# Performance work log

Measured on AMD Instinct MI355X. Metric: run time of the kernel, lower is better.

## Reference

```python
import jax, jax.numpy as jnp
import numpy as np

N_HEADS = 8
WINDOW = 7

def _conv1x1(x, W, b):
    # x: [B,H,W,C]; 1x1 conv == per-pixel matmul
    return jnp.einsum('bhwc,cd->bhwd', x, W) + b

def _to_heads(t, nh):
    # [B,H,W,C] -> channels-first reshape [B, nh, C//nh, H*W] (matches tf transpose+reshape)
    B, H, W, C = t.shape
    return jnp.transpose(t, (0, 3, 1, 2)).reshape(B, nh, C // nh, H * W)

def setup_inputs() -> dict:
    key = jax.random.key(0)
    ks = jax.random.split(key, 8)
    B, H, W, C = 2, 56, 56, 256
    x = jax.random.normal(ks[0], (B, H, W, C), dtype=jnp.float32)
    s = 1.0 / np.sqrt(C)
    Wq = jax.random.normal(ks[1], (C, C), dtype=jnp.float32) * s
    bq = jnp.zeros((C,), dtype=jnp.float32)
    Wk = jax.random.normal(ks[2], (C, C), dtype=jnp.float32) * s
    bk = jnp.zeros((C,), dtype=jnp.float32)
    Wv = jax.random.normal(ks[3], (C, C), dtype=jnp.float32) * s
    bv = jnp.zeros((C,), dtype=jnp.float32)
    # original initializes gamma to 0 (output == x); use small nonzero so the
    # attention path is observable in outputs/grads
    gamma = jax.random.normal(ks[4], (1,), dtype=jnp.float32) * 0.1
    return {"x": x, "Wq": Wq, "bq": bq, "Wk": Wk, "bk": bk, "Wv": Wv, "bv": bv, "gamma": gamma}

def reference(x, Wq, bq, Wk, bk, Wv, bv, gamma):
    B, H, W, C = x.shape
    p = WINDOW // 2
    xp = jnp.pad(x, ((0, 0), (p, p), (p, p), (0, 0)), mode='reflect')  # [B,Hp,Wp,C]
    q = _to_heads(_conv1x1(x, Wq, bq), N_HEADS)    # [B,nh,dk,HW]
    k = _to_heads(_conv1x1(xp, Wk, bk), N_HEADS)   # [B,nh,dk,HpWp]
    v = _to_heads(_conv1x1(xp, Wv, bv), N_HEADS)   # [B,nh,dk,HpWp]
    energy = jnp.einsum('bhdq,bhdk->bhqk', q, k)   # [B,nh,HW,HpWp]
    attn = jax.nn.softmax(energy, axis=-1)
    out = jnp.einsum('bhdk,bhqk->bhdq', v, attn)   # [B,nh,dk,HW]
    out = out.reshape(B, C, H, W).transpose(0, 2, 3, 1)
    return gamma * out + x
```

## Files before the change

### kernel.cpp

```cpp
#include <hip/hip_runtime.h>

typedef unsigned short u16;
typedef float f32x4 __attribute__((ext_vector_type(4)));
typedef short bf16x8 __attribute__((ext_vector_type(8)));

__device__ __forceinline__ u16 f2bf(float f) {
    unsigned u = __float_as_uint(f);
    u = (u + 0x7FFFu + ((u >> 16) & 1u)) >> 16;
    return (u16)u;
}

#define LOG2E 1.4426950408889634f

#if __has_builtin(__builtin_amdgcn_exp2f)
__device__ __forceinline__ float exp2_fast(float x) { return __builtin_amdgcn_exp2f(x); }
#else
__device__ __forceinline__ float exp2_fast(float x) { return __expf(x * 0.6931471805599453f); }
#endif

__device__ __forceinline__ unsigned pack2bf(float a, float b) {
    unsigned ua = __float_as_uint(a) + 0x8000u;
    unsigned ub = __float_as_uint(b) + 0x8000u;
#if __has_builtin(__builtin_amdgcn_perm)
    return __builtin_amdgcn_perm(ub, ua, 0x07060302u);
#else
    return ((ua >> 16) & 0xFFFFu) | (ub & 0xFFFF0000u);
#endif
}

#if __has_builtin(__builtin_amdgcn_cvt_pk_bf16_f32)
typedef __bf16 bf2_t __attribute__((ext_vector_type(2)));
__device__ __forceinline__ unsigned cvtpk(float a, float b) {
    bf2_t r = __builtin_amdgcn_cvt_pk_bf16_f32(a, b);
    return __builtin_bit_cast(unsigned, r);
}
#else
__device__ __forceinline__ unsigned cvtpk(float a, float b) { return pack2bf(a, b); }
#endif

__device__ __forceinline__ bf16x8 bc8(uint4 u) { return __builtin_bit_cast(bf16x8, u); }

#if __has_builtin(__builtin_amdgcn_global_load_lds)
typedef const __attribute__((address_space(1))) void* as1cv;
typedef __attribute__((address_space(3))) void* as3v;
__device__ __forceinline__ void dma16(const void* g, void* lds_base, int lane) {
    __builtin_amdgcn_global_load_lds((as1cv)g, (as3v)lds_base, 16, 0, 0);
}
#else
__device__ __forceinline__ void dma16(const void* g, void* lds_base, int lane) {
    *(uint4*)((char*)lds_base + lane * 16) = *(const uint4*)g;
}
#endif

#define BB 2
#define HH 56
#define SQ 3136
#define CROWN 3584

#define WS_Q    0
#define WS_K    1605632
#define WS_V    3244032
#define WS_WT   4882432
#define WS_CB   5079040
#define WS_XB   5082624

__global__ __launch_bounds__(256) void prep_kernel(const float* __restrict__ x,
                                                   const float* __restrict__ Wq,
                                                   const float* __restrict__ Wk,
                                                   const float* __restrict__ Wv,
                                                   u16* __restrict__ wtf,
                                                   u16* __restrict__ kbf,
                                                   u16* __restrict__ vbf,
                                                   u16* __restrict__ crow,
                                                   u16* __restrict__ xbf) {
    __shared__ __align__(16) char SM[17408];
    int tid = threadIdx.x;
    int bid = blockIdx.x;

    if (bid < 48) {
        u16 (*T)[68] = (u16(*)[68])SM;
        int mode = bid >> 4, rem = bid & 15;
        int kx = (rem >> 2) * 64, dx = (rem & 3) * 64;
        const float* W = (mode == 0) ? Wq : ((mode == 1) ? Wk : Wv);
        float sc = (mode == 0) ? LOG2E : 1.0f;
        int r16 = tid >> 4, c4 = (tid & 15) * 4;
#pragma unroll
        for (int p = 0; p < 4; ++p) {
            int kr = p * 16 + r16;
            float4 f = *(const float4*)&W[(size_t)(kx + kr) * 256 + dx + c4];
            T[kr][c4 + 0] = f2bf(f.x * sc);
            T[kr][c4 + 1] = f2bf(f.y * sc);
            T[kr][c4 + 2] = f2bf(f.z * sc);
            T[kr][c4 + 3] = f2bf(f.w * sc);
        }
        __syncthreads();
        int l16 = tid & 15, nt_loc = (tid >> 4) & 3, quad = (tid >> 6) & 3;
#pragma unroll
        for (int s_loc = 0; s_loc < 2; ++s_loc) {
            int k0 = s_loc * 32 + quad * 8;
            int d_loc = nt_loc * 16 + l16;
            u16 tmp[8];
#pragma unroll
            for (int j = 0; j < 8; ++j) tmp[j] = T[k0 + j][d_loc];
            int d = dx + d_loc;
            int nz = d >> 7, ntg = (d >> 4) & 7;
            int s = (kx >> 5) + s_loc;
            int f = (nz * 8 + s) * 8 + ntg;
            int L = quad * 16 + l16;
            *(uint4*)&wtf[(size_t)mode * 65536 + (size_t)f * 512 + (size_t)L * 8] = *(uint4*)tmp;
        }
        uint4 z4 = (uint4){0, 0, 0, 0};
        if (mode == 0 && kx == 0 && dx == 0) {
            for (int i = tid; i < 4096; i += 256) {
                int bb = i >> 11, rem2 = i & 2047;
                int t = 196 + (rem2 >> 9), off = (rem2 & 511) * 8;
                *(uint4*)&kbf[(((size_t)(bb * 200 + t)) << 12) + off] = z4;
            }
        }
        if (mode == 1 && kx == 0 && dx == 0) {
            for (int i = tid; i < CROWN; i += 256) {
                u16 v = 0;
                if (i < SQ) {
                    int rr = i / 56, cc = i - rr * 56;
                    int mr = (((rr >= 1) && (rr <= 3)) || ((rr >= 52) && (rr <= 54))) ? 2 : 1;
                    int mc = (((cc >= 1) && (cc <= 3)) || ((cc >= 52) && (cc <= 54))) ? 2 : 1;
                    int prod = mr * mc;
                    v = (prod == 1) ? (u16)0x3F80 : ((prod == 2) ? (u16)0x4000 : (u16)0x4080);
                }
                crow[i] = v;
            }
        }
        if (mode == 2 && kx == 0 && dx == 0) {
            for (int i = tid; i < 8192; i += 256) {
                int bh = i >> 9, rem2 = i & 511;
                int wp = rem2 >> 7, rem3 = rem2 & 127;
                int vh = rem3 >> 6, ln = rem3 & 63;
                size_t off = (size_t)bh * 102400 + (size_t)(96 + wp) * 1024
                           + (size_t)vh * 512 + (size_t)ln * 8 + 4;
                *(uint2*)&vbf[off] = (uint2){0, 0};
            }
        }
    } else {
        float (*T)[256] = (float(*)[256])SM;
        int tile = bid - 48;
        int r = tid >> 4, c0 = (tid & 15) * 16;
        const float* src = x + ((size_t)tile * 16 + r) * 256 + c0;
#pragma unroll
        for (int k = 0; k < 4; ++k)
            *(float4*)&T[r][c0 + k * 4] = *(const float4*)&src[k * 4];
        __syncthreads();
#pragma unroll
        for (int e = 0; e < 2; ++e) {
            int g = tid + e * 256;
            int s = g >> 6, L = g & 63;
            const float* row = &T[L & 15][s * 32 + (L >> 4) * 8];
            uint4 pk = (uint4){pack2bf(row[0], row[1]), pack2bf(row[2], row[3]),
                               pack2bf(row[4], row[5]), pack2bf(row[6], row[7])};
            *(uint4*)&xbf[(size_t)tile * 4096 + (size_t)g * 8] = pk;
        }
    }
}

__global__ __launch_bounds__(256, 4) void proj_kernel(const u16* __restrict__ xbf,
                                                      const u16* __restrict__ wtf,
                                                      const float* __restrict__ bq,
                                                      const float* __restrict__ bk,
                                                      const float* __restrict__ bv,
                                                      u16* __restrict__ qbf,
                                                      u16* __restrict__ kbf,
                                                      u16* __restrict__ vbf) {
    int mode = blockIdx.y, nz = blockIdx.z;
    int mbase = blockIdx.x * 64;
    int tid = threadIdx.x;
    int wave = tid >> 6, lane = tid & 63, quad = (tid >> 4) & 3, l16 = tid & 15;
    const float* bias = (mode == 0) ? bq : ((mode == 1) ? bk : bv);
    float wsc = (mode == 0) ? LOG2E : 1.0f;
    const u16* wf = wtf + (size_t)mode * 65536 + (size_t)nz * 32768 + (size_t)lane * 8;
    const u16* xt = xbf + (((size_t)(mbase >> 4) + wave) << 12);

    f32x4 acc[8];
#pragma unroll
    for (int i = 0; i < 8; i++) acc[i] = (f32x4){0.f, 0.f, 0.f, 0.f};

#pragma unroll
    for (int s = 0; s < 8; ++s) {
        bf16x8 af = *(const bf16x8*)&xt[(s << 9) + lane * 8];
        if (mode == 2) {
#pragma unroll
            for (int nt = 0; nt < 8; nt++) {
                bf16x8 bfrag = *(const bf16x8*)&wf[(s * 8 + nt) * 512];
                acc[nt] = __builtin_amdgcn_mfma_f32_16x16x32_bf16(af, bfrag, acc[nt], 0, 0, 0);
            }
        } else {
#pragma unroll
            for (int nt = 0; nt < 8; nt++) {
                bf16x8 bfrag = *(const bf16x8*)&wf[(s * 8 + nt) * 512];
                acc[nt] = __builtin_amdgcn_mfma_f32_16x16x32_bf16(bfrag, af, acc[nt], 0, 0, 0);
            }
        }
    }

    if (mode == 2) {
        int b_ = (mbase >= SQ) ? 1 : 0;
        int kp0 = mbase - b_ * SQ + wave * 16 + quad * 4;
        int rg = (mbase - b_ * SQ + wave * 16) >> 4;
        int ch = rg >> 3, wp = rg & 3, which = (rg >> 2) & 1;
        float mult[4];
#pragma unroll
        for (int p = 0; p < 4; ++p) {
            int kp = kp0 + p;
            int rr = kp / 56, cc = kp - rr * 56;
            float mr = (((rr >= 1) && (rr <= 3)) || ((rr >= 52) && (rr <= 54))) ? 2.f : 1.f;
            float mc = (((cc >= 1) && (cc <= 3)) || ((cc >= 52) && (cc <= 54))) ? 2.f : 1.f;
            mult[p] = mr * mc;
        }
#pragma unroll
        for (int nt = 0; nt < 8; nt++) {
            int c = nz * 128 + nt * 16 + l16;
            float bvv = bias[c];
            int h_idx = nz * 4 + (nt >> 1);
            int bh2 = b_ * 8 + h_idx;
            float va0 = (acc[nt][0] + bvv) * mult[0];
            float va1 = (acc[nt][1] + bvv) * mult[1];
            float va2 = (acc[nt][2] + bvv) * mult[2];
            float va3 = (acc[nt][3] + bvv) * mult[3];
            uint2 pk = (uint2){pack2bf(va0, va1), pack2bf(va2, va3)};
            size_t off = (size_t)bh2 * 102400 + (size_t)(ch * 4 + wp) * 1024
                       + (size_t)(nt & 1) * 512 + (size_t)(quad * 16 + l16) * 8 + which * 4;
            *(uint2*)&vbf[off] = pk;
        }
    } else {
        u16* outp = (mode == 0) ? qbf : kbf;
        int t = (mbase >> 4) + wave;
        int tt = (mode == 0) ? t : (t + (t >= 196 ? 4 : 0));
#pragma unroll
        for (int nt = 0; nt < 8; nt++) {
            int c0 = nz * 128 + nt * 16 + quad * 4;
            float4 b4 = *(const float4*)&bias[c0];
            float v0 = acc[nt][0] + b4.x * wsc;
            float v1 = acc[nt][1] + b4.y * wsc;
            float v2 = acc[nt][2] + b4.z * wsc;
            float v3 = acc[nt][3] + b4.w * wsc;
            int s_idx = nz * 4 + (nt >> 1);
            int Lrow = ((nt & 1) * 2 + (quad >> 1)) * 16 + l16;
            uint2 pk = (uint2){pack2bf(v0, v1), pack2bf(v2, v3)};
            *(uint2*)&outp[(((size_t)(tt * 8 + s_idx)) << 9) + Lrow * 8 + (quad & 1) * 4] = pk;
        }
    }
}

__global__ __launch_bounds__(256, 4) void attn_kernel(const u16* __restrict__ qb,
                                                      const u16* __restrict__ kb,
                                                      const u16* __restrict__ vtb,
                                                      const u16* __restrict__ crow,
                                                      const float* __restrict__ x,
                                                      const float* __restrict__ gammap,
                                                      float* __restrict__ out) {
    __shared__ __align__(16) u16 S[19968];

    int tid = threadIdx.x;
    int w = tid >> 6, lane = tid & 63, quad = lane >> 4, l16 = lane & 15;
    int bh = blockIdx.x;
    int b = bh >> 3, h = bh & 7;
    int qsub = blockIdx.y * 64;

    int qtile = b * 196 + blockIdx.y * 4;
    bf16x8 qf[4];
#pragma unroll
    for (int i = 0; i < 4; ++i)
        qf[i] = *(const bf16x8*)&qb[(((size_t)(qtile + i) * 8 + h) << 9) + lane * 8];

    const u16* kg = kb + ((size_t)(b * 200) << 12);
    const u16* vg = vtb + (size_t)bh * 102400;

    f32x4 o[4][2], lv[4];
#pragma unroll
    for (int i = 0; i < 4; ++i) {
        o[i][0] = (f32x4){0.f, 0.f, 0.f, 0.f};
        o[i][1] = (f32x4){0.f, 0.f, 0.f, 0.f};
        lv[i]   = (f32x4){0.f, 0.f, 0.f, 0.f};
    }

    int tA = w, tB = w + 4;
    auto stage = [&](int r_ch, int buf) {
        u16* base = &S[buf * 8192];
        int rgA = r_ch * 8 + tA, rgB = r_ch * 8 + tB;
        dma16(kg + (((size_t)rgA * 8 + h) << 9) + lane * 8, base + tA * 512, lane);
        dma16(kg + (((size_t)rgB * 8 + h) << 9) + lane * 8, base + tB * 512, lane);
        const u16* vsrc = vg + (size_t)r_ch * 4096 + w * 1024;
        dma16(vsrc + lane * 8, base + 4096 + w * 1024, lane);
        dma16(vsrc + 512 + lane * 8, base + 4096 + w * 1024 + 512, lane);
    };

    int kOffA = tA * 512 + lane * 8;
    int kOffB = tB * 512 + lane * 8;
    int vOff  = 4096 + w * 1024 + lane * 8;
    int cOffA = tA * 16 + quad * 4;
    int cOffB = tB * 16 + quad * 4;

    auto round_body = [&](int r, int bR) {
        const u16* Kl = &S[bR * 8192];
        const u16* cnt = &S[16384] + r * 128;
        f32x4 z = (f32x4){0.f, 0.f, 0.f, 0.f};
        unsigned paw[4][4];

        {
            bf16x8 kfA = *(const bf16x8*)&Kl[kOffA];
            f32x4 eA[4];
            __builtin_amdgcn_s_setprio(1);
#pragma unroll
            for (int i = 0; i < 4; ++i)
                eA[i] = __builtin_amdgcn_mfma_f32_16x16x32_bf16(kfA, qf[i], z, 0, 0, 0);
            __builtin_amdgcn_s_setprio(0);
#pragma unroll
            for (int i = 0; i < 4; ++i) {
                paw[i][0] = cvtpk(exp2_fast(eA[i][0]), exp2_fast(eA[i][1]));
                paw[i][1] = cvtpk(exp2_fast(eA[i][2]), exp2_fast(eA[i][3]));
            }
        }
        {
            bf16x8 kfB = *(const bf16x8*)&Kl[kOffB];
            f32x4 eB[4];
            __builtin_amdgcn_s_setprio(1);
#pragma unroll
            for (int i = 0; i < 4; ++i)
                eB[i] = __builtin_amdgcn_mfma_f32_16x16x32_bf16(kfB, qf[i], z, 0, 0, 0);
            __builtin_amdgcn_s_setprio(0);
#pragma unroll
            for (int i = 0; i < 4; ++i) {
                paw[i][2] = cvtpk(exp2_fast(eB[i][0]), exp2_fast(eB[i][1]));
                paw[i][3] = cvtpk(exp2_fast(eB[i][2]), exp2_fast(eB[i][3]));
            }
        }
        uint2 ca = *(const uint2*)&cnt[cOffA];
        uint2 cc = *(const uint2*)&cnt[cOffB];
        bf16x8 cf = bc8((uint4){ca.x, ca.y, cc.x, cc.y});
        bf16x8 V0 = *(const bf16x8*)&Kl[vOff];
        bf16x8 V1 = *(const bf16x8*)&Kl[vOff + 512];

        __builtin_amdgcn_s_setprio(1);
#pragma unroll
        for (int i = 0; i < 4; ++i) {
            bf16x8 pa = bc8((uint4){paw[i][0], paw[i][1], paw[i][2], paw[i][3]});
            o[i][0] = __builtin_amdgcn_mfma_f32_16x16x32_bf16(pa, V0, o[i][0], 0, 0, 0);
            o[i][1] = __builtin_amdgcn_mfma_f32_16x16x32_bf16(pa, V1, o[i][1], 0, 0, 0);
            lv[i]   = __builtin_amdgcn_mfma_f32_16x16x32_bf16(pa, cf, lv[i], 0, 0, 0);
        }
        __builtin_amdgcn_s_setprio(0);
    };

    {
        dma16(crow + w * 512 + lane * 8, (char*)&S[16384] + w * 1024, lane);
        if (w + 4 < 7)
            dma16(crow + (w + 4) * 512 + lane * 8, (char*)&S[16384] + (w + 4) * 1024, lane);
    }
    stage(0, 0);
    __syncthreads();

    for (int r = 0; r < 25; ++r) {
        if (r + 1 < 25) {
            stage(r + 1, (r + 1) & 1);
            asm volatile("s_waitcnt vmcnt(4)" ::: "memory");
        } else {
            asm volatile("s_waitcnt vmcnt(0)" ::: "memory");
        }
        round_body(r, r & 1);
    }
    __syncthreads();

    float* mg = (float*)&S[0];
    {
        int slot = ((w & 1) * 64 + lane) * 48;
        if (w >= 2) {
#pragma unroll
            for (int i = 0; i < 4; ++i) {
                *(f32x4*)&mg[slot + i * 8]      = o[i][0];
                *(f32x4*)&mg[slot + i * 8 + 4]  = o[i][1];
                *(f32x4*)&mg[slot + 32 + i * 4] = lv[i];
            }
        }
        __syncthreads();
        if (w < 2) {
#pragma unroll
            for (int i = 0; i < 4; ++i) {
                o[i][0] += *(const f32x4*)&mg[slot + i * 8];
                o[i][1] += *(const f32x4*)&mg[slot + i * 8 + 4];
                lv[i]   += *(const f32x4*)&mg[slot + 32 + i * 4];
            }
        }
        __syncthreads();
    }
    {
        int slot = lane * 48;
        if (w == 1) {
#pragma unroll
            for (int i = 0; i < 4; ++i) {
                *(f32x4*)&mg[slot + i * 8]      = o[i][0];
                *(f32x4*)&mg[slot + i * 8 + 4]  = o[i][1];
                *(f32x4*)&mg[slot + 32 + i * 4] = lv[i];
            }
        }
        __syncthreads();
        if (w == 0) {
            float gam = gammap[0];
#pragma unroll
            for (int i = 0; i < 4; ++i) {
                o[i][0] += *(const f32x4*)&mg[slot + i * 8];
                o[i][1] += *(const f32x4*)&mg[slot + i * 8 + 4];
                lv[i]   += *(const f32x4*)&mg[slot + 32 + i * 4];
#pragma unroll
                for (int r2 = 0; r2 < 4; ++r2) {
                    float scl = gam / lv[i][r2];
                    int q = qsub + i * 16 + quad * 4 + r2;
                    size_t base = ((size_t)(b * SQ + q) << 8) + h * 32 + l16;
                    out[base]      = o[i][0][r2] * scl + x[base];
                    out[base + 16] = o[i][1][r2] * scl + x[base + 16];
                }
            }
        }
    }
}

extern "C" void kernel_launch(void* const* d_in, const int* in_sizes, int n_in,
                              void* d_out, int out_size, void* d_ws, size_t ws_size,
                              hipStream_t stream) {
    const float* x     = (const float*)d_in[0];
    const float* Wq    = (const float*)d_in[1];
    const float* bq    = (const float*)d_in[2];
    const float* Wk    = (const float*)d_in[3];
    const float* bk    = (const float*)d_in[4];
    const float* Wv    = (const float*)d_in[5];
    const float* bv    = (const float*)d_in[6];
    const float* gamma = (const float*)d_in[7];
    float* out = (float*)d_out;

    u16* ws   = (u16*)d_ws;
    u16* qbf  = ws + WS_Q;
    u16* kbf  = ws + WS_K;
    u16* vbf  = ws + WS_V;
    u16* wtf  = ws + WS_WT;
    u16* crow = ws + WS_CB;
    u16* xbf  = ws + WS_XB;

    prep_kernel<<<440, 256, 0, stream>>>(x, Wq, Wk, Wv, wtf, kbf, vbf, crow, xbf);
    proj_kernel<<<dim3(98, 3, 2), 256, 0, stream>>>(xbf, wtf, bq, bk, bv, qbf, kbf, vbf);
    attn_kernel<<<dim3(16, 49), 256, 0, stream>>>(qbf, kbf, vbf, crow, x, gamma, out);
}
```

Measured before the change: 128.6 us.

## Halve attention query tile, load V directly to registers, raise occupancy

The attention kernel now processes 32 queries per block instead of 64, doubling the grid to 98 query blocks per head. V tiles are loaded straight from global memory into registers instead of staged through LDS, which shrinks shared memory use and lets launch bounds ask for 7 blocks per CU. The main loop is unrolled by two with explicit double buffering, and the last round uses a count fragment held in registers. This targets more parallelism and latency hiding, at the cost of reloading K/V twice as often across blocks and more global traffic.

New measurement: 211.6 us. +64.5%, slower.

```diff
diff --git a/kernel.cpp b/kernel.cpp
--- a/kernel.cpp
+++ b/kernel.cpp
@@ -249,98 +249,100 @@
     }
 }
 
-__global__ __launch_bounds__(256, 4) void attn_kernel(const u16* __restrict__ qb,
+__global__ __launch_bounds__(256, 7) void attn_kernel(const u16* __restrict__ qb,
                                                       const u16* __restrict__ kb,
                                                       const u16* __restrict__ vtb,
                                                       const u16* __restrict__ crow,
                                                       const float* __restrict__ x,
                                                       const float* __restrict__ gammap,
                                                       float* __restrict__ out) {
-    __shared__ __align__(16) u16 S[19968];
+    __shared__ __align__(16) u16 S[11264];
 
     int tid = threadIdx.x;
     int w = tid >> 6, lane = tid & 63, quad = lane >> 4, l16 = lane & 15;
     int bh = blockIdx.x;
     int b = bh >> 3, h = bh & 7;
-    int qsub = blockIdx.y * 64;
-
-    int qtile = b * 196 + blockIdx.y * 4;
-    bf16x8 qf[4];
-#pragma unroll
-    for (int i = 0; i < 4; ++i)
+    int qy = blockIdx.y;
+    int qsub = qy * 32;
+
+    int qtile = b * 196 + qy * 2;
+    bf16x8 qf[2];
+#pragma unroll
+    for (int i = 0; i < 2; ++i)
         qf[i] = *(const bf16x8*)&qb[(((size_t)(qtile + i) * 8 + h) << 9) + lane * 8];
 
     const u16* kg = kb + ((size_t)(b * 200) << 12);
     const u16* vg = vtb + (size_t)bh * 102400;
 
-    f32x4 o[4][2], lv[4];
-#pragma unroll
-    for (int i = 0; i < 4; ++i) {
+    f32x4 o[2][2], lv[2];
+#pragma unroll
+    for (int i = 0; i < 2; ++i) {
         o[i][0] = (f32x4){0.f, 0.f, 0.f, 0.f};
         o[i][1] = (f32x4){0.f, 0.f, 0.f, 0.f};
         lv[i]   = (f32x4){0.f, 0.f, 0.f, 0.f};
     }
 
     int tA = w, tB = w + 4;
-    auto stage = [&](int r_ch, int buf) {
-        u16* base = &S[buf * 8192];
-        int rgA = r_ch * 8 + tA, rgB = r_ch * 8 + tB;
-        dma16(kg + (((size_t)rgA * 8 + h) << 9) + lane * 8, base + tA * 512, lane);
-        dma16(kg + (((size_t)rgB * 8 + h) << 9) + lane * 8, base + tB * 512, lane);
-        const u16* vsrc = vg + (size_t)r_ch * 4096 + w * 1024;
-        dma16(vsrc + lane * 8, base + 4096 + w * 1024, lane);
-        dma16(vsrc + 512 + lane * 8, base + 4096 + w * 1024 + 512, lane);
-    };
-
     int kOffA = tA * 512 + lane * 8;
     int kOffB = tB * 512 + lane * 8;
-    int vOff  = 4096 + w * 1024 + lane * 8;
     int cOffA = tA * 16 + quad * 4;
     int cOffB = tB * 16 + quad * 4;
 
-    auto round_body = [&](int r, int bR) {
-        const u16* Kl = &S[bR * 8192];
-        const u16* cnt = &S[16384] + r * 128;
+    uint2 ca24 = *(const uint2*)&crow[3072 + cOffA];
+
+    auto stageK = [&](int r, int buf) {
+        u16* base = &S[buf * 4096];
+        dma16(kg + (((size_t)((r * 8 + tA) * 8 + h)) << 9) + lane * 8, base + tA * 512, lane);
+        dma16(kg + (((size_t)((r * 8 + tB) * 8 + h)) << 9) + lane * 8, base + tB * 512, lane);
+    };
+    auto loadV = [&](int r, uint4& v0, uint4& v1) {
+        const u16* vsrc = vg + (size_t)r * 4096 + w * 1024 + lane * 8;
+        v0 = *(const uint4*)&vsrc[0];
+        v1 = *(const uint4*)&vsrc[512];
+    };
+    auto cfLDS = [&](int r) -> bf16x8 {
+        const u16* cnt = &S[8192 + r * 128];
+        uint2 ca = *(const uint2*)&cnt[cOffA];
+        uint2 cc = *(const uint2*)&cnt[cOffB];
+        return bc8((uint4){ca.x, ca.y, cc.x, cc.y});
+    };
+
+    auto body = [&](int bR, uint4 v0, uint4 v1, bf16x8 cf) {
+        const u16* Kl = &S[bR * 4096];
         f32x4 z = (f32x4){0.f, 0.f, 0.f, 0.f};
-        unsigned paw[4][4];
-
+        unsigned paw[2][4];
         {
             bf16x8 kfA = *(const bf16x8*)&Kl[kOffA];
-            f32x4 eA[4];
+            f32x4 eA[2];
             __builtin_amdgcn_s_setprio(1);
 #pragma unroll
-            for (int i = 0; i < 4; ++i)
+            for (int i = 0; i < 2; ++i)
                 eA[i] = __builtin_amdgcn_mfma_f32_16x16x32_bf16(kfA, qf[i], z, 0, 0, 0);
             __builtin_amdgcn_s_setprio(0);
 #pragma unroll
-            for (int i = 0; i < 4; ++i) {
+            for (int i = 0; i < 2; ++i) {
                 paw[i][0] = cvtpk(exp2_fast(eA[i][0]), exp2_fast(eA[i][1]));
                 paw[i][1] = cvtpk(exp2_fast(eA[i][2]), exp2_fast(eA[i][3]));
             }
         }
         {
             bf16x8 kfB = *(const bf16x8*)&Kl[kOffB];
-            f32x4 eB[4];
+            f32x4 eB[2];
             __builtin_amdgcn_s_setprio(1);
 #pragma unroll
-            for (int i = 0; i < 4; ++i)
+            for (int i = 0; i < 2; ++i)
                 eB[i] = __builtin_amdgcn_mfma_f32_16x16x32_bf16(kfB, qf[i], z, 0, 0, 0);
             __builtin_amdgcn_s_setprio(0);
 #pragma unroll
-            for (int i = 0; i < 4; ++i) {
+            for (int i = 0; i < 2; ++i) {
                 paw[i][2] = cvtpk(exp2_fast(eB[i][0]), exp2_fast(eB[i][1]));
                 paw[i][3] = cvtpk(exp2_fast(eB[i][2]), exp2_fast(eB[i][3]));
             }
         }
-        uint2 ca = *(const uint2*)&cnt[cOffA];
-        uint2 cc = *(const uint2*)&cnt[cOffB];
-        bf16x8 cf = bc8((uint4){ca.x, ca.y, cc.x, cc.y});
-        bf16x8 V0 = *(const bf16x8*)&Kl[vOff];
-        bf16x8 V1 = *(const bf16x8*)&Kl[vOff + 512];
-
+        bf16x8 V0 = bc8(v0), V1 = bc8(v1);
         __builtin_amdgcn_s_setprio(1);
 #pragma unroll
-        for (int i = 0; i < 4; ++i) {
+        for (int i = 0; i < 2; ++i) {
             bf16x8 pa = bc8((uint4){paw[i][0], paw[i][1], paw[i][2], paw[i][3]});
             o[i][0] = __builtin_amdgcn_mfma_f32_16x16x32_bf16(pa, V0, o[i][0], 0, 0, 0);
             o[i][1] = __builtin_amdgcn_mfma_f32_16x16x32_bf16(pa, V1, o[i][1], 0, 0, 0);
@@ -349,65 +351,73 @@
         __builtin_amdgcn_s_setprio(0);
     };
 
-    {
-        dma16(crow + w * 512 + lane * 8, (char*)&S[16384] + w * 1024, lane);
-        if (w + 4 < 7)
-            dma16(crow + (w + 4) * 512 + lane * 8, (char*)&S[16384] + (w + 4) * 1024, lane);
-    }
-    stage(0, 0);
+    dma16(crow + w * 512 + lane * 8, (char*)&S[8192] + w * 1024, lane);
+    if (w < 2)
+        dma16(crow + (w + 4) * 512 + lane * 8, (char*)&S[8192] + (w + 4) * 1024, lane);
+    stageK(0, 0);
+    uint4 va0, va1, vb0, vb1;
+    loadV(0, va0, va1);
     __syncthreads();
 
-    for (int r = 0; r < 25; ++r) {
-        if (r + 1 < 25) {
-            stage(r + 1, (r + 1) & 1);
-            asm volatile("s_waitcnt vmcnt(4)" ::: "memory");
-        } else {
-            asm volatile("s_waitcnt vmcnt(0)" ::: "memory");
-        }
-        round_body(r, r & 1);
-    }
+    for (int j = 0; j < 12; ++j) {
+        int r = 2 * j;
+        stageK(r + 1, 1);
+        loadV(r + 1, vb0, vb1);
+        asm volatile("s_waitcnt vmcnt(4)" ::: "memory");
+        body(0, va0, va1, cfLDS(r));
+        stageK(r + 2, 0);
+        loadV(r + 2, va0, va1);
+        asm volatile("s_waitcnt vmcnt(4)" ::: "memory");
+        body(1, vb0, vb1, cfLDS(r + 1));
+    }
+    asm volatile("s_waitcnt vmcnt(0)" ::: "memory");
+    body(0, va0, va1, bc8((uint4){ca24.x, ca24.y, 0u, 0u}));
+
     __syncthreads();
 
     float* mg = (float*)&S[0];
     {
-        int slot = ((w & 1) * 64 + lane) * 48;
+        int slot = ((w & 1) * 64 + lane) * 24;
         if (w >= 2) {
-#pragma unroll
-            for (int i = 0; i < 4; ++i) {
-                *(f32x4*)&mg[slot + i * 8]      = o[i][0];
-                *(f32x4*)&mg[slot + i * 8 + 4]  = o[i][1];
-                *(f32x4*)&mg[slot + 32 + i * 4] = lv[i];
-            }
+            *(f32x4*)&mg[slot + 0]  = o[0][0];
+            *(f32x4*)&mg[slot + 4]  = o[0][1];
+            *(f32x4*)&mg[slot + 8]  = o[1][0];
+            *(f32x4*)&mg[slot + 12] = o[1][1];
+            *(f32x4*)&mg[slot + 16] = lv[0];
+            *(f32x4*)&mg[slot + 20] = lv[1];
         }
         __syncthreads();
         if (w < 2) {
-#pragma unroll
-            for (int i = 0; i < 4; ++i) {
-                o[i][0] += *(const f32x4*)&mg[slot + i * 8];
-                o[i][1] += *(const f32x4*)&mg[slot + i * 8 + 4];
-                lv[i]   += *(const f32x4*)&mg[slot + 32 + i * 4];
-            }
+            o[0][0] += *(const f32x4*)&mg[slot + 0];
+            o[0][1] += *(const f32x4*)&mg[slot + 4];
+            o[1][0] += *(const f32x4*)&mg[slot + 8];
+            o[1][1] += *(const f32x4*)&mg[slot + 12];
+            lv[0]   += *(const f32x4*)&mg[slot + 16];
+            lv[1]   += *(const f32x4*)&mg[slot + 20];
         }
         __syncthreads();
     }
     {
-        int slot = lane * 48;
+        int slot = lane * 24;
         if (w == 1) {
-#pragma unroll
-            for (int i = 0; i < 4; ++i) {
-                *(f32x4*)&mg[slot + i * 8]      = o[i][0];
-                *(f32x4*)&mg[slot + i * 8 + 4]  = o[i][1];
-                *(f32x4*)&mg[slot + 32 + i * 4] = lv[i];
-            }
+            *(f32x4*)&mg[slot + 0]  = o[0][0];
+            *(f32x4*)&mg[slot + 4]  = o[0][1];
+            *(f32x4*)&mg[slot + 8]  = o[1][0];
+            *(f32x4*)&mg[slot + 12] = o[1][1];
+            *(f32x4*)&mg[slot + 16] = lv[0];
+            *(f32x4*)&mg[slot + 20] = lv[1];
         }
         __syncthreads();
         if (w == 0) {
             float gam = gammap[0];
-#pragma unroll
-            for (int i = 0; i < 4; ++i) {
-                o[i][0] += *(const f32x4*)&mg[slot + i * 8];
-                o[i][1] += *(const f32x4*)&mg[slot + i * 8 + 4];
-                lv[i]   += *(const f32x4*)&mg[slot + 32 + i * 4];
+            o[0][0] += *(const f32x4*)&mg[slot + 0];
+            o[0][1] += *(const f32x4*)&mg[slot + 4];
+            o[1][0] += *(const f32x4*)&mg[slot + 8];
+            o[1][1] += *(const f32x4*)&mg[slot + 12];
+            lv[0]   += *(const f32x4*)&mg[slot + 16];
+            lv[1]   += *(const f32x4*)&mg[slot + 20];
+#pragma unroll
+            for (int i = 0; i < 2; ++i) {
 #pragma unroll
                 for (int r2 = 0; r2 < 4; ++r2) {
                     float scl = gam / lv[i][r2];
@@ -444,5 +454,5 @@
 
     prep_kernel<<<440, 256, 0, stream>>>(x, Wq, Wk, Wv, wtf, kbf, vbf, crow, xbf);
     proj_kernel<<<dim3(98, 3, 2), 256, 0, stream>>>(xbf, wtf, bq, bk, bv, qbf, kbf, vbf);
-    attn_kernel<<<dim3(16, 49), 256, 0, stream>>>(qbf, kbf, vbf, crow, x, gamma, out);
-}
+    attn_kernel<<<dim3(16, 98), 256, 0, stream>>>(qbf, kbf, vbf, crow, x, gamma, out);
+}
```
